# Optimization experiments

Hardware: AMD Instinct MI355X
Metric: run time of the kernel (lower is better)

## Reference

```python
import jax, jax.numpy as jnp
import numpy as np

RANK = 16
ALPHA = 16.0
SCALING = ALPHA / RANK
N_ADAPTERS = 8
IN_F = 4096
OUT_F = 4096
BATCH = 4
SEQ = 2048


def setup_inputs() -> dict:
    key = jax.random.key(0)
    kx, ka, kb, ki = jax.random.split(key, 4)
    x = jax.random.normal(kx, (BATCH, SEQ, IN_F), dtype=jnp.float32)
    # A init: randn * 0.02 (as in module). B is zeros in the module; use small
    # random values here so the baseline output/grads are non-trivial.
    A = jax.random.normal(ka, (N_ADAPTERS, OUT_F, RANK), dtype=jnp.float32) * 0.02
    B = jax.random.normal(kb, (N_ADAPTERS, RANK, IN_F), dtype=jnp.float32) * 0.02
    adapter_ids = jax.random.randint(ki, (BATCH,), 0, N_ADAPTERS, dtype=jnp.int32)
    return {"x": x, "A": A, "B": B, "adapter_ids": adapter_ids}


def reference(x, A, B, adapter_ids):
    # Original: Bx = einsum('bni,ari->bnar', x, B); res = einsum('bnar,aor->bnao', Bx, A)
    # then res[arange(b), :, adapter_ids] * scaling.
    # Equivalent (gather-then-batched-GEMM): select each batch element's adapter
    # first, avoiding the O(n_adapters) dense intermediate. Same math.
    B_sel = B[adapter_ids]            # [b, r, in]
    A_sel = A[adapter_ids]            # [b, out, r]
    Bx = jnp.einsum('bni,bri->bnr', x, B_sel)   # [b, n, r]
    out = jnp.einsum('bnr,bor->bno', Bx, A_sel)  # [b, n, out]
    return out * SCALING
```

## Files before the change

### kernel.cpp

```cpp
#include <hip/hip_runtime.h>
#include <hip/hip_bf16.h>

#define RANK   16
#define IN_F   4096
#define OUT_F  4096
#define SEQLEN 2048
#define NROWS  8192

typedef __bf16 bf16x8   __attribute__((ext_vector_type(8)));
typedef float  floatx4  __attribute__((ext_vector_type(4)));
typedef float  floatx16 __attribute__((ext_vector_type(16)));

static __device__ __forceinline__ bf16x8 cvt8(floatx4 a, floatx4 b) {
    bf16x8 r;
    r[0] = (__bf16)a[0]; r[1] = (__bf16)a[1]; r[2] = (__bf16)a[2]; r[3] = (__bf16)a[3];
    r[4] = (__bf16)b[0]; r[5] = (__bf16)b[1]; r[6] = (__bf16)b[2]; r[7] = (__bf16)b[3];
    return r;
}

__global__ __launch_bounds__(512, 4) void
lora_fused_kernel(const float* __restrict__ x, const float* __restrict__ Aw,
                  const float* __restrict__ Bw, const int* __restrict__ ids,
                  float* __restrict__ out)
{
    const int tile = blockIdx.x;
    const int row0 = tile * 16;
    const int adapter = ids[row0 >> 11];
    const int tid  = threadIdx.x;
    const int wave = tid >> 6;
    const int lane = tid & 63;

    __shared__ float  red[8][256];
    __shared__ __bf16 bxs[256];

    {
        const int m    = lane & 15;
        const int quad = lane >> 4;
        const int k0   = wave * 512 + quad * 8;
        const float* xp = x + (size_t)(row0 + m) * IN_F + k0;
        const float* bp = Bw + (size_t)adapter * (RANK * IN_F) + m * IN_F + k0;

        floatx4 acc = {0.f, 0.f, 0.f, 0.f};
#pragma unroll
        for (int s = 0; s < 16; ++s) {
            floatx4 xa = *reinterpret_cast<const floatx4*>(xp + s * 32);
            floatx4 xb = *reinterpret_cast<const floatx4*>(xp + s * 32 + 4);
            floatx4 ba = *reinterpret_cast<const floatx4*>(bp + s * 32);
            floatx4 bb = *reinterpret_cast<const floatx4*>(bp + s * 32 + 4);
            acc = __builtin_amdgcn_mfma_f32_16x16x32_bf16(
                cvt8(xa, xb), cvt8(ba, bb), acc, 0, 0, 0);
        }
#pragma unroll
        for (int j = 0; j < 4; ++j)
            red[wave][(quad * 4 + j) * 16 + m] = acc[j];
    }
    __syncthreads();
    if (tid < 256) {
        float s = ((red[0][tid] + red[1][tid]) + (red[2][tid] + red[3][tid]))
                + ((red[4][tid] + red[5][tid]) + (red[6][tid] + red[7][tid]));
        bxs[tid] = (__bf16)s;
    }
    __syncthreads();

    {
        const int n    = lane & 31;
        const int half = lane >> 5;
        const int mm   = n & 15;

        const bf16x8 a_bx = *reinterpret_cast<const bf16x8*>(bxs + mm * 16 + half * 8);
        const float* ap = Aw + (size_t)adapter * (OUT_F * RANK) + half * 8;

#pragma unroll 4
        for (int t = 0; t < 16; ++t) {
            const int col0 = (wave * 16 + t) * 32;
            floatx4 fa = *reinterpret_cast<const floatx4*>(ap + (size_t)(col0 + n) * RANK);
            floatx4 fb = *reinterpret_cast<const floatx4*>(ap + (size_t)(col0 + n) * RANK + 4);
            floatx16 c;
#pragma unroll
            for (int i = 0; i < 16; ++i) c[i] = 0.f;
            c = __builtin_amdgcn_mfma_f32_32x32x16_bf16(a_bx, cvt8(fa, fb), c, 0, 0, 0);
#pragma unroll
            for (int reg = 0; reg < 8; ++reg) {
                const int r = (reg & 3) + 8 * (reg >> 2) + 4 * half;
                __builtin_nontemporal_store(
                    c[reg], out + (size_t)(row0 + r) * OUT_F + col0 + n);
            }
        }
    }
}

extern "C" void kernel_launch(void* const* d_in, const int* in_sizes, int n_in,
                              void* d_out, int out_size, void* d_ws, size_t ws_size,
                              hipStream_t stream) {
    const float* x   = (const float*)d_in[0];
    const float* Aw  = (const float*)d_in[1];
    const float* Bw  = (const float*)d_in[2];
    const int*   ids = (const int*)d_in[3];
    float* out = (float*)d_out;

    lora_fused_kernel<<<dim3(NROWS / 16), dim3(512), 0, stream>>>(x, Aw, Bw, ids, out);
}
```

Baseline: 249.7 us.

## Split fused LoRA kernel into Bx projection and output expansion kernels

Splits the single fused kernel into two launches. The first computes the rank-16 Bx projection per 16-row tile and writes it to a bf16 workspace. The second spreads the output expansion over four times as many smaller blocks and uses a 16x16x32 MFMA whose result is written as 128-bit stores instead of scalar nontemporal stores. This aims for more parallelism and better store coalescing in the write-heavy output phase, at the cost of an extra launch, a workspace round-trip, and half of each MFMA being zero-padded.

```diff
diff --git a/kernel.cpp b/kernel.cpp
--- a/kernel.cpp
+++ b/kernel.cpp
@@ -4,12 +4,10 @@
 #define RANK   16
 #define IN_F   4096
 #define OUT_F  4096
-#define SEQLEN 2048
 #define NROWS  8192
 
 typedef __bf16 bf16x8   __attribute__((ext_vector_type(8)));
 typedef float  floatx4  __attribute__((ext_vector_type(4)));
-typedef float  floatx16 __attribute__((ext_vector_type(16)));
 
 static __device__ __forceinline__ bf16x8 cvt8(floatx4 a, floatx4 b) {
     bf16x8 r;
@@ -19,9 +17,8 @@
 }
 
 __global__ __launch_bounds__(512, 4) void
-lora_fused_kernel(const float* __restrict__ x, const float* __restrict__ Aw,
-                  const float* __restrict__ Bw, const int* __restrict__ ids,
-                  float* __restrict__ out)
+lora_bx_kernel(const float* __restrict__ x, const float* __restrict__ Bw,
+               const int* __restrict__ ids, __bf16* __restrict__ bx)
 {
     const int tile = blockIdx.x;
     const int row0 = tile * 16;
@@ -30,62 +27,76 @@
     const int wave = tid >> 6;
     const int lane = tid & 63;
 
-    __shared__ float  red[8][256];
-    __shared__ __bf16 bxs[256];
+    __shared__ float red[8][256];
 
-    {
-        const int m    = lane & 15;
-        const int quad = lane >> 4;
-        const int k0   = wave * 512 + quad * 8;
-        const float* xp = x + (size_t)(row0 + m) * IN_F + k0;
-        const float* bp = Bw + (size_t)adapter * (RANK * IN_F) + m * IN_F + k0;
+    const int m    = lane & 15;
+    const int quad = lane >> 4;
+    const int k0   = wave * 512 + quad * 8;
+    const float* xp = x + (size_t)(row0 + m) * IN_F + k0;
+    const float* bp = Bw + (size_t)adapter * (RANK * IN_F) + m * IN_F + k0;
 
-        floatx4 acc = {0.f, 0.f, 0.f, 0.f};
+    floatx4 acc = {0.f, 0.f, 0.f, 0.f};
 #pragma unroll
-        for (int s = 0; s < 16; ++s) {
-            floatx4 xa = *reinterpret_cast<const floatx4*>(xp + s * 32);
-            floatx4 xb = *reinterpret_cast<const floatx4*>(xp + s * 32 + 4);
-            floatx4 ba = *reinterpret_cast<const floatx4*>(bp + s * 32);
-            floatx4 bb = *reinterpret_cast<const floatx4*>(bp + s * 32 + 4);
-            acc = __builtin_amdgcn_mfma_f32_16x16x32_bf16(
-                cvt8(xa, xb), cvt8(ba, bb), acc, 0, 0, 0);
-        }
+    for (int s = 0; s < 16; ++s) {
+        floatx4 xa = *reinterpret_cast<const floatx4*>(xp + s * 32);
+        floatx4 xb = *reinterpret_cast<const floatx4*>(xp + s * 32 + 4);
+        floatx4 ba = *reinterpret_cast<const floatx4*>(bp + s * 32);
+        floatx4 bb = *reinterpret_cast<const floatx4*>(bp + s * 32 + 4);
+        acc = __builtin_amdgcn_mfma_f32_16x16x32_bf16(
+            cvt8(xa, xb), cvt8(ba, bb), acc, 0, 0, 0);
+    }
 #pragma unroll
-        for (int j = 0; j < 4; ++j)
-            red[wave][(quad * 4 + j) * 16 + m] = acc[j];
-    }
+    for (int j = 0; j < 4; ++j)
+        red[wave][(quad * 4 + j) * 16 + m] = acc[j];
     __syncthreads();
     if (tid < 256) {
         float s = ((red[0][tid] + red[1][tid]) + (red[2][tid] + red[3][tid]))
                 + ((red[4][tid] + red[5][tid]) + (red[6][tid] + red[7][tid]));
-        bxs[tid] = (__bf16)s;
+        bx[tile * 256 + tid] = (__bf16)s;
     }
-    __syncthreads();
+}
 
-    {
-        const int n    = lane & 31;
-        const int half = lane >> 5;
-        const int mm   = n & 15;
+__global__ __launch_bounds__(256, 8) void
+lora_out_kernel(const float* __restrict__ Aw, const __bf16* __restrict__ bx,
+                const int* __restrict__ ids, float* __restrict__ out)
+{
+    const int blk      = blockIdx.x;
+    const int row_tile = blk >> 2;
+    const int ochunk   = blk & 3;
+    const int row0     = row_tile * 16;
+    const int adapter  = ids[row0 >> 11];
+    const int tid  = threadIdx.x;
+    const int wave = tid >> 6;
+    const int lane = tid & 63;
+    const int rl   = lane & 15;
+    const int quad = lane >> 4;
 
-        const bf16x8 a_bx = *reinterpret_cast<const bf16x8*>(bxs + mm * 16 + half * 8);
-        const float* ap = Aw + (size_t)adapter * (OUT_F * RANK) + half * 8;
+    bf16x8 zfrag;
+#pragma unroll
+    for (int i = 0; i < 8; ++i) zfrag[i] = (__bf16)0.f;
+
+    bf16x8 bfrag = zfrag;
+    if (quad < 2)
+        bfrag = *reinterpret_cast<const bf16x8*>(bx + row0 * 16 + rl * 16 + quad * 8);
+
+    const float* ap = Aw + (size_t)adapter * (OUT_F * RANK);
+    const int o_base = ochunk * 1024 + wave * 256;
 
 #pragma unroll 4
-        for (int t = 0; t < 16; ++t) {
-            const int col0 = (wave * 16 + t) * 32;
-            floatx4 fa = *reinterpret_cast<const floatx4*>(ap + (size_t)(col0 + n) * RANK);
-            floatx4 fb = *reinterpret_cast<const floatx4*>(ap + (size_t)(col0 + n) * RANK + 4);
-            floatx16 c;
-#pragma unroll
-            for (int i = 0; i < 16; ++i) c[i] = 0.f;
-            c = __builtin_amdgcn_mfma_f32_32x32x16_bf16(a_bx, cvt8(fa, fb), c, 0, 0, 0);
-#pragma unroll
-            for (int reg = 0; reg < 8; ++reg) {
-                const int r = (reg & 3) + 8 * (reg >> 2) + 4 * half;
-                __builtin_nontemporal_store(
-                    c[reg], out + (size_t)(row0 + r) * OUT_F + col0 + n);
-            }
+    for (int t = 0; t < 16; ++t) {
+        const int o0 = o_base + t * 16;
+        bf16x8 afrag = zfrag;
+        if (quad < 2) {
+            floatx4 fa = *reinterpret_cast<const floatx4*>(
+                ap + (size_t)(o0 + rl) * RANK + quad * 8);
+            floatx4 fb = *reinterpret_cast<const floatx4*>(
+                ap + (size_t)(o0 + rl) * RANK + quad * 8 + 4);
+            afrag = cvt8(fa, fb);
         }
+        floatx4 c = {0.f, 0.f, 0.f, 0.f};
+        c = __builtin_amdgcn_mfma_f32_16x16x32_bf16(afrag, bfrag, c, 0, 0, 0);
+        *reinterpret_cast<floatx4*>(
+            out + (size_t)(row0 + rl) * OUT_F + o0 + quad * 4) = c;
     }
 }
 
@@ -98,5 +109,8 @@
     const int*   ids = (const int*)d_in[3];
     float* out = (float*)d_out;
 
-    lora_fused_kernel<<<dim3(NROWS / 16), dim3(512), 0, stream>>>(x, Aw, Bw, ids, out);
+    __bf16* bxws = (__bf16*)d_ws;
+
+    lora_bx_kernel<<<dim3(NROWS / 16), dim3(512), 0, stream>>>(x, Bw, ids, bxws);
+    lora_out_kernel<<<dim3(2048), dim3(256), 0, stream>>>(Aw, bxws, ids, out);
 }
```

Result: slower. 285.2 us (+14.2%).

## Stage x and B through double-buffered LDS with async global-to-LDS loads

Applied to the files above, without the earlier changes.

Phase one now streams x and B in 256-wide K chunks into double-buffered shared memory using global_load_lds. The next chunk is prefetched while the current one is computed, replacing direct strided per-lane global loads. Block-to-tile mapping is swizzled across the grid. The output phase switches to a 16x16x32 MFMA with zero-padded fragments so each lane issues 16-byte vector stores instead of scalar ones. The costs are two barriers per chunk and much more LDS use, which can lower occupancy.

```diff
diff --git a/kernel.cpp b/kernel.cpp
--- a/kernel.cpp
+++ b/kernel.cpp
@@ -4,12 +4,14 @@
 #define RANK   16
 #define IN_F   4096
 #define OUT_F  4096
-#define SEQLEN 2048
 #define NROWS  8192
+#define NTILES (NROWS / 16)
+#define CK     256
+#define NC     (IN_F / CK)
+#define LDSP   260
 
-typedef __bf16 bf16x8   __attribute__((ext_vector_type(8)));
-typedef float  floatx4  __attribute__((ext_vector_type(4)));
-typedef float  floatx16 __attribute__((ext_vector_type(16)));
+typedef __bf16 bf16x8  __attribute__((ext_vector_type(8)));
+typedef float  floatx4 __attribute__((ext_vector_type(4)));
 
 static __device__ __forceinline__ bf16x8 cvt8(floatx4 a, floatx4 b) {
     bf16x8 r;
@@ -18,42 +20,75 @@
     return r;
 }
 
+static __device__ __forceinline__ void stage16(const float* g, float* l) {
+    __builtin_amdgcn_global_load_lds(
+        (const __attribute__((address_space(1))) void*)g,
+        (__attribute__((address_space(3))) void*)l, 16, 0, 0);
+}
+
 __global__ __launch_bounds__(512, 4) void
-lora_fused_kernel(const float* __restrict__ x, const float* __restrict__ Aw,
-                  const float* __restrict__ Bw, const int* __restrict__ ids,
-                  float* __restrict__ out)
+lora_fused2_kernel(const float* __restrict__ x, const float* __restrict__ Aw,
+                   const float* __restrict__ Bw, const int* __restrict__ ids,
+                   float* __restrict__ out)
 {
-    const int tile = blockIdx.x;
+    const int b    = blockIdx.x;
+    const int tile = (b & 7) * (NTILES / 8) + (b >> 3);
     const int row0 = tile * 16;
     const int adapter = ids[row0 >> 11];
     const int tid  = threadIdx.x;
     const int wave = tid >> 6;
     const int lane = tid & 63;
+    const int m    = lane & 15;
+    const int quad = lane >> 4;
 
+    __shared__ float  xs [2][16][LDSP];
+    __shared__ float  bsh[2][16][LDSP];
     __shared__ float  red[8][256];
     __shared__ __bf16 bxs[256];
 
-    {
-        const int m    = lane & 15;
-        const int quad = lane >> 4;
-        const int k0   = wave * 512 + quad * 8;
-        const float* xp = x + (size_t)(row0 + m) * IN_F + k0;
-        const float* bp = Bw + (size_t)adapter * (RANK * IN_F) + m * IN_F + k0;
+    const float* xrow = x  + (size_t)(row0 + 2 * wave) * IN_F + lane * 4;
+    const float* brow = Bw + ((size_t)adapter * RANK + 2 * wave) * IN_F + lane * 4;
 
-        floatx4 acc = {0.f, 0.f, 0.f, 0.f};
+    auto STAGE = [&](int c, int bf) {
+        const float* xsrc = xrow + c * CK;
+        const float* bsrc = brow + c * CK;
+        stage16(xsrc,        &xs [bf][2 * wave    ][0]);
+        stage16(xsrc + IN_F, &xs [bf][2 * wave + 1][0]);
+        stage16(bsrc,        &bsh[bf][2 * wave    ][0]);
+        stage16(bsrc + IN_F, &bsh[bf][2 * wave + 1][0]);
+    };
+
+    floatx4 acc = {0.f, 0.f, 0.f, 0.f};
+    const int koff = wave * 32 + quad * 8;
+
+    auto COMPUTE = [&](int bf) {
+        floatx4 xa = *reinterpret_cast<const floatx4*>(&xs [bf][m][koff]);
+        floatx4 xb = *reinterpret_cast<const floatx4*>(&xs [bf][m][koff + 4]);
+        floatx4 ba = *reinterpret_cast<const floatx4*>(&bsh[bf][m][koff]);
+        floatx4 bb = *reinterpret_cast<const floatx4*>(&bsh[bf][m][koff + 4]);
+        acc = __builtin_amdgcn_mfma_f32_16x16x32_bf16(
+            cvt8(xa, xb), cvt8(ba, bb), acc, 0, 0, 0);
+    };
+
+    STAGE(0, 0);
+    int bf = 0;
+    for (int c = 0; c < NC - 1; ++c) {
+        STAGE(c + 1, bf ^ 1);
+        asm volatile("s_waitcnt vmcnt(4)" ::: "memory");
+        __builtin_amdgcn_sched_barrier(0);
+        __syncthreads();
+        COMPUTE(bf);
+        __syncthreads();
+        bf ^= 1;
+    }
+    asm volatile("s_waitcnt vmcnt(0)" ::: "memory");
+    __builtin_amdgcn_sched_barrier(0);
+    __syncthreads();
+    COMPUTE(bf);
+
 #pragma unroll
-        for (int s = 0; s < 16; ++s) {
-            floatx4 xa = *reinterpret_cast<const floatx4*>(xp + s * 32);
-            floatx4 xb = *reinterpret_cast<const floatx4*>(xp + s * 32 + 4);
-            floatx4 ba = *reinterpret_cast<const floatx4*>(bp + s * 32);
-            floatx4 bb = *reinterpret_cast<const floatx4*>(bp + s * 32 + 4);
-            acc = __builtin_amdgcn_mfma_f32_16x16x32_bf16(
-                cvt8(xa, xb), cvt8(ba, bb), acc, 0, 0, 0);
-        }
-#pragma unroll
-        for (int j = 0; j < 4; ++j)
-            red[wave][(quad * 4 + j) * 16 + m] = acc[j];
-    }
+    for (int j = 0; j < 4; ++j)
+        red[wave][(quad * 4 + j) * 16 + m] = acc[j];
     __syncthreads();
     if (tid < 256) {
         float s = ((red[0][tid] + red[1][tid]) + (red[2][tid] + red[3][tid]))
@@ -62,30 +97,33 @@
     }
     __syncthreads();
 
-    {
-        const int n    = lane & 31;
-        const int half = lane >> 5;
-        const int mm   = n & 15;
+    bf16x8 zfrag;
+#pragma unroll
+    for (int i = 0; i < 8; ++i) zfrag[i] = (__bf16)0.f;
 
-        const bf16x8 a_bx = *reinterpret_cast<const bf16x8*>(bxs + mm * 16 + half * 8);
-        const float* ap = Aw + (size_t)adapter * (OUT_F * RANK) + half * 8;
+    bf16x8 bfrag = zfrag;
+    if (quad < 2)
+        bfrag = *reinterpret_cast<const bf16x8*>(bxs + m * 16 + quad * 8);
+
+    const float* ap = Aw + (size_t)adapter * (OUT_F * RANK);
+    const int o_base = wave * 512;
 
 #pragma unroll 4
-        for (int t = 0; t < 16; ++t) {
-            const int col0 = (wave * 16 + t) * 32;
-            floatx4 fa = *reinterpret_cast<const floatx4*>(ap + (size_t)(col0 + n) * RANK);
-            floatx4 fb = *reinterpret_cast<const floatx4*>(ap + (size_t)(col0 + n) * RANK + 4);
-            floatx16 c;
-#pragma unroll
-            for (int i = 0; i < 16; ++i) c[i] = 0.f;
-            c = __builtin_amdgcn_mfma_f32_32x32x16_bf16(a_bx, cvt8(fa, fb), c, 0, 0, 0);
-#pragma unroll
-            for (int reg = 0; reg < 8; ++reg) {
-                const int r = (reg & 3) + 8 * (reg >> 2) + 4 * half;
-                __builtin_nontemporal_store(
-                    c[reg], out + (size_t)(row0 + r) * OUT_F + col0 + n);
-            }
+    for (int t = 0; t < 32; ++t) {
+        const int o0 = o_base + t * 16;
+        bf16x8 afrag = zfrag;
+        if (quad < 2) {
+            floatx4 fa = *reinterpret_cast<const floatx4*>(
+                ap + (size_t)(o0 + m) * RANK + quad * 8);
+            floatx4 fb = *reinterpret_cast<const floatx4*>(
+                ap + (size_t)(o0 + m) * RANK + quad * 8 + 4);
+            afrag = cvt8(fa, fb);
         }
+        floatx4 c4 = {0.f, 0.f, 0.f, 0.f};
+        c4 = __builtin_amdgcn_mfma_f32_16x16x32_bf16(afrag, bfrag, c4, 0, 0, 0);
+        __builtin_nontemporal_store(
+            c4, reinterpret_cast<floatx4*>(
+                    out + (size_t)(row0 + m) * OUT_F + o0 + quad * 4));
     }
 }
 
@@ -98,5 +136,5 @@
     const int*   ids = (const int*)d_in[3];
     float* out = (float*)d_out;
 
-    lora_fused_kernel<<<dim3(NROWS / 16), dim3(512), 0, stream>>>(x, Aw, Bw, ids, out);
+    lora_fused2_kernel<<<dim3(NTILES), dim3(512), 0, stream>>>(x, Aw, Bw, ids, out);
 }
```

Measured after the change: 263.2 us. 5.4% more time.
